# Kernel tuning notes

Measured on AMD Instinct MI355X. Metric: run time of the kernel, lower is better.

Reference implementation:

```python
import jax, jax.numpy as jnp
import numpy as np

B, DIM, NX, NY = 4, 64, 256, 256
HEADS, DIM_HEAD, LATENT, DIM_OUT, KM = 4, 32, 128, 64, 2
DH = DIM_HEAD * KM  # LowRankKernel head dim (also RoPE dim) = 64
EPS = 1e-5
MIN_FREQ = 1.0 / 64.0  # RotaryEmbedding default in FactFormer/LNS repo


def _gelu(x):
    return jax.nn.gelu(x, approximate=False)  # torch nn.GELU default (erf)


def _conv1x1(u, w):
    # u: [b,c,h,w], w: [out,c]  (1x1 conv == channel matmul)
    return jnp.einsum('bchw,oc->bohw', u, w)


def _pooling_reducer(x, win, ln_g, ln_b, w1, w2, b2):
    # x: [b, n_keep, n_pool, c] -> Linear, mean-pool over n_pool, LN+FFN
    h = jnp.einsum('bnmc,hc->bnmh', x, win).mean(axis=2)  # [b, n, hid]
    m = h.mean(axis=-1, keepdims=True)
    v = h.var(axis=-1, keepdims=True)
    h = (h - m) / jnp.sqrt(v + EPS) * ln_g + ln_b
    return _gelu(h @ w1.T) @ w2.T + b2  # [b, n, latent]


def _rope_freqs(n):
    pos = jnp.linspace(0.0, 1.0, n) / MIN_FREQ  # scale/min_freq = 64
    inv = 1.0 / (10000.0 ** (jnp.arange(0, DH, 2, dtype=jnp.float32) / DH))
    f = pos[:, None] * inv[None, :]            # [n, DH//2]
    return jnp.concatenate([f, f], axis=-1)    # [n, DH]


def _apply_rope(x, f):
    # rotate_half = cat(-x2, x1) on half-split (FactFormer convention)
    d = x.shape[-1] // 2
    rot = jnp.concatenate([-x[..., d:], x[..., :d]], axis=-1)
    return x * jnp.cos(f) + rot * jnp.sin(f)


def _low_rank_kernel(x, wqk):
    # x: [b, n, latent] -> K: [b, heads, n, n]; scaling=1, dropout=Identity, qk_norm=False
    b, n, _ = x.shape
    qk = x @ wqk.T
    q, k = jnp.split(qk, 2, axis=-1)
    q = q.reshape(b, n, HEADS, DH).transpose(0, 2, 1, 3)
    k = k.reshape(b, n, HEADS, DH).transpose(0, 2, 1, 3)
    f = _rope_freqs(n)
    q = _apply_rope(q, f)
    k = _apply_rope(k, f)
    return jnp.einsum('bhid,bhjd->bhij', q, k)


def _forward(u, gn_w, gn_b, w_in_proj, w_to_in,
             px_win, px_ln_g, px_ln_b, px_w1, px_w2, px_b2,
             py_win, py_ln_g, py_ln_b, py_w1, py_w2, py_b2,
             kx_wqk, ky_wqk, out_w1, out_w2):
    # GroupNorm(1, dim): normalize over (C,H,W) per sample, affine
    m = u.mean(axis=(1, 2, 3), keepdims=True)
    v = u.var(axis=(1, 2, 3), keepdims=True)
    un = (u - m) / jnp.sqrt(v + EPS) * gn_w[None, :, None, None] + gn_b[None, :, None, None]
    u_phi = _conv1x1(un, w_in_proj)  # [b, heads*dim_head, nx, ny]
    ui = _conv1x1(un, w_to_in)       # [b, dim, nx, ny]
    # to_x: pool over ny -> tokens along nx; to_y: pool over nx -> tokens along ny
    ux = _pooling_reducer(ui.transpose(0, 2, 3, 1), px_win, px_ln_g, px_ln_b, px_w1, px_w2, px_b2)  # [b, nx, latent]
    uy = _pooling_reducer(ui.transpose(0, 3, 2, 1), py_win, py_ln_g, py_ln_b, py_w1, py_w2, py_b2)  # [b, ny, latent]
    kx = _low_rank_kernel(ux, kx_wqk)  # [b, h, nx, nx]
    ky = _low_rank_kernel(uy, ky_wqk)  # [b, h, ny, ny]
    b, hc, nx, ny = u_phi.shape
    up = u_phi.reshape(b, HEADS, hc // HEADS, nx, ny)
    up = jnp.einsum('bhij,bhcjm->bhcim', kx, up)
    up = jnp.einsum('bhlm,bhcim->bhcil', ky, up)
    up = up.reshape(b, hc, nx, ny)
    # InstanceNorm2d (no affine, no running stats)
    m2 = up.mean(axis=(2, 3), keepdims=True)
    v2 = up.var(axis=(2, 3), keepdims=True)
    upn = (up - m2) / jnp.sqrt(v2 + EPS)
    out = _conv1x1(_gelu(_conv1x1(upn, out_w1)), out_w2)
    return out + u


def setup_inputs() -> dict:
    key = jax.random.key(0)
    ks = jax.random.split(key, 16)
    def w(k, shape, s=0.02):
        return (jax.random.normal(k, shape) * s).astype(jnp.float32)
    return {
        'u': jax.random.normal(ks[0], (B, DIM, NX, NY), dtype=jnp.float32),
        'gn_w': jnp.ones((DIM,), jnp.float32), 'gn_b': jnp.zeros((DIM,), jnp.float32),
        'w_in_proj': w(ks[1], (HEADS * DIM_HEAD, DIM)),
        'w_to_in': w(ks[2], (DIM, DIM)),
        'px_win': w(ks[3], (DIM, DIM)),
        'px_ln_g': jnp.ones((DIM,), jnp.float32), 'px_ln_b': jnp.zeros((DIM,), jnp.float32),
        'px_w1': w(ks[4], (2 * DIM, DIM)), 'px_w2': w(ks[5], (LATENT, 2 * DIM)),
        'px_b2': jnp.zeros((LATENT,), jnp.float32),
        'py_win': w(ks[6], (DIM, DIM)),
        'py_ln_g': jnp.ones((DIM,), jnp.float32), 'py_ln_b': jnp.zeros((DIM,), jnp.float32),
        'py_w1': w(ks[7], (2 * DIM, DIM)), 'py_w2': w(ks[8], (LATENT, 2 * DIM)),
        'py_b2': jnp.zeros((LATENT,), jnp.float32),
        'kx_wqk': w(ks[9], (2 * HEADS * DH, LATENT)),
        'ky_wqk': w(ks[10], (2 * HEADS * DH, LATENT)),
        'out_w1': w(ks[11], (DIM_OUT, HEADS * DIM_HEAD)),
        'out_w2': w(ks[12], (DIM_OUT, DIM_OUT)),
    }


def reference(u, gn_w, gn_b, w_in_proj, w_to_in,
              px_win, px_ln_g, px_ln_b, px_w1, px_w2, px_b2,
              py_win, py_ln_g, py_ln_b, py_w1, py_w2, py_b2,
              kx_wqk, ky_wqk, out_w1, out_w2):
    return _forward(u, gn_w, gn_b, w_in_proj, w_to_in,
                    px_win, px_ln_g, px_ln_b, px_w1, px_w2, px_b2,
                    py_win, py_ln_g, py_ln_b, py_w1, py_w2, py_b2,
                    kx_wqk, ky_wqk, out_w1, out_w2)
```

## Files before the change

kernel.cpp:

```cpp
#include <hip/hip_runtime.h>
#include <math.h>

typedef unsigned short ushort_t;
typedef unsigned int uint_t;
typedef __attribute__((ext_vector_type(8))) short s8v;
typedef __attribute__((ext_vector_type(4))) float f4;

#define NPIX 65536
#define EPS_ 1e-5f

__device__ __forceinline__ float bf2f(ushort_t u){ return __uint_as_float(((uint_t)u)<<16); }
__device__ __forceinline__ ushort_t f2bf(float f){
  uint_t u = __float_as_uint(f);
  uint_t r = (u + 0x7fffu + ((u>>16)&1u)) >> 16;
  return (ushort_t)r;
}
__device__ __forceinline__ float bflo(uint_t p){ return __uint_as_float(p<<16); }
__device__ __forceinline__ float bfhi(uint_t p){ return __uint_as_float(p & 0xffff0000u); }
__device__ __forceinline__ uint_t packbf(float a, float b){ return (uint_t)f2bf(a) | ((uint_t)f2bf(b)<<16); }

__device__ __forceinline__ f4 MFMA(s8v a, s8v b, f4 c){
  return __builtin_amdgcn_mfma_f32_16x16x32_bf16(a, b, c, 0, 0, 0);
}

__device__ __forceinline__ float wave_sum(float v){
  #pragma unroll
  for(int m=32;m>=1;m>>=1) v += __shfl_xor(v, m, 64);
  return v;
}

__global__ __launch_bounds__(256) void k1_stats(const float* __restrict__ u,
    float* __restrict__ part, float* __restrict__ pc, float* __restrict__ poolx){
  int blk = blockIdx.x; int b = blk>>8; int c = (blk>>2)&63; int iq = blk&3;
  int t = threadIdx.x; int lane = t&63; int w = t>>6;
  const float* up = u + ((size_t)(b*64+c))*NPIX + iq*64*256;
  __shared__ float sCol[4][256];
  __shared__ float red[8];
  float4 cs4 = {0.f,0.f,0.f,0.f};
  float ss = 0.f;
  #pragma unroll 4
  for(int r16=0;r16<16;r16++){
    int r = w*16 + r16;
    float4 v = *(const float4*)(up + r*256 + lane*4);
    cs4.x+=v.x; cs4.y+=v.y; cs4.z+=v.z; cs4.w+=v.w;
    ss += v.x*v.x+v.y*v.y+v.z*v.z+v.w*v.w;
    float rs = wave_sum(v.x+v.y+v.z+v.w);
    if(lane==0) poolx[(b*256 + iq*64 + r)*64 + c] = rs*(1.f/256.f);
  }
  *(float4*)&sCol[w][lane*4] = cs4;
  float ssw = wave_sum(ss);
  if(lane==0) red[w] = ssw;
  __syncthreads();
  float colsum = sCol[0][t]+sCol[1][t]+sCol[2][t]+sCol[3][t];
  pc[((b*64+c)*4+iq)*256 + t] = colsum;
  float s1 = wave_sum(colsum);
  if(lane==0) red[4+w] = s1;
  __syncthreads();
  if(t==0){
    part[((b*64+c)*4+iq)*2]   = red[4]+red[5]+red[6]+red[7];
    part[((b*64+c)*4+iq)*2+1] = red[0]+red[1]+red[2]+red[3];
  }
}

__global__ void k2_fin(const float* __restrict__ part, float* __restrict__ gnmv){
  int t = threadIdx.x; int b = t>>6; int i = t&63;
  float S1=0.f, S2=0.f;
  #pragma unroll
  for(int q=0;q<4;q++){
    S1 += part[((b*64+i)*4+q)*2];
    S2 += part[((b*64+i)*4+q)*2+1];
  }
  S1 = wave_sum(S1); S2 = wave_sum(S2);
  if(i==0){
    const float inv = 1.f/4194304.f;
    float m = S1*inv; float v = S2*inv - m*m;
    gnmv[b*2] = m; gnmv[b*2+1] = rsqrtf(v + EPS_);
  }
}

__global__ __launch_bounds__(256) void k8a_fold(const float* __restrict__ gnmv,
    const float* __restrict__ gnw, const float* __restrict__ gnb,
    const float* __restrict__ w_in_proj, const float* __restrict__ out_w2,
    ushort_t* __restrict__ wpb, float* __restrict__ c0g, ushort_t* __restrict__ w2b){
  int b = blockIdx.x; int t = threadIdx.x;
  __shared__ float scs[64], shs[64];
  if(t<64){
    float mean = gnmv[b*2], rstd = gnmv[b*2+1];
    float sc = rstd*gnw[t];
    scs[t] = sc; shs[t] = gnb[t] - mean*sc;
  }
  __syncthreads();
  int oc = t>>1, h = t&1;
  float c0 = 0.f;
  for(int k=0;k<32;k++){
    int ch = h*32 + k;
    float wv = w_in_proj[oc*64 + ch];
    wpb[((size_t)b*128 + oc)*64 + ch] = f2bf(wv*scs[ch]);
    c0 += wv*shs[ch];
  }
  c0 += __shfl_xor(c0, 1, 64);
  if(h==0) c0g[b*128 + oc] = c0;
  if(b==0){
    for(int e=t;e<4096;e+=256) w2b[e] = f2bf(out_w2[e]);
  }
}

__global__ void k8b_fold(const float* __restrict__ istat,
    const float* __restrict__ out_w1, ushort_t* __restrict__ W1b,
    float* __restrict__ bias1){
  int b = blockIdx.x; int t = threadIdx.x;
  __shared__ float ms[128], rss[128];
  ms[t] = istat[(b*128+t)*2];       rss[t] = istat[(b*128+t)*2+1];
  ms[64+t] = istat[(b*128+64+t)*2]; rss[64+t] = istat[(b*128+64+t)*2+1];
  __syncthreads();
  float bias = 0.f;
  for(int ch=0;ch<128;ch++){
    float wv = out_w1[t*128 + ch];
    float wr = wv*rss[ch];
    W1b[((size_t)b*64 + t)*128 + ch] = f2bf(wr);
    bias += wr*ms[ch];
  }
  bias1[b*64 + t] = bias;
}

__global__ __launch_bounds__(128) void k3_reduce(
    const float* __restrict__ poolx, const float* __restrict__ pc,
    const float* __restrict__ gnmv,
    const float* __restrict__ gnw, const float* __restrict__ gnb,
    const float* __restrict__ w_to_in,
    const float* __restrict__ xwin, const float* __restrict__ xlg, const float* __restrict__ xlb,
    const float* __restrict__ xw1, const float* __restrict__ xw2, const float* __restrict__ xb2,
    const float* __restrict__ ywin, const float* __restrict__ ylg, const float* __restrict__ ylb,
    const float* __restrict__ yw1, const float* __restrict__ yw2, const float* __restrict__ yb2,
    float* __restrict__ ux, float* __restrict__ uy){
  int id = blockIdx.x;
  int side = id >> 10; int r = id & 1023; int b = r>>8; int i = r&255;
  const float* win = side ? ywin : xwin;
  const float* lg  = side ? ylg  : xlg;
  const float* lb  = side ? ylb  : xlb;
  const float* w1  = side ? yw1  : xw1;
  const float* w2  = side ? yw2  : xw2;
  const float* b2  = side ? yb2  : xb2;
  float* outp = side ? uy : ux;
  int t = threadIdx.x;
  __shared__ float pn[64], t1[64], hh[64], f1[128];
  float mean = gnmv[b*2], rstd = gnmv[b*2+1];
  if(t<64){
    float pv;
    if(side){
      const float* p = pc + ((size_t)(b*64+t)*4)*256 + i;
      pv = (p[0] + p[256] + p[512] + p[768]) * (1.f/256.f);
    } else {
      pv = poolx[(b*256+i)*64 + t];
    }
    pn[t] = (pv - mean)*rstd*gnw[t] + gnb[t];
  }
  __syncthreads();
  if(t<64){
    float acc=0.f; const float* wr = w_to_in + t*64;
    #pragma unroll 8
    for(int c=0;c<64;c++) acc += pn[c]*wr[c];
    t1[t]=acc;
  }
  __syncthreads();
  if(t<64){
    float acc=0.f; const float* wr = win + t*64;
    #pragma unroll 8
    for(int c=0;c<64;c++) acc += t1[c]*wr[c];
    hh[t]=acc;
  }
  __syncthreads();
  if(t<64){
    float v = hh[t];
    float s = wave_sum(v);
    float ss = wave_sum(v*v);
    float m2 = s*(1.f/64.f);
    float var = ss*(1.f/64.f) - m2*m2;
    float rs2 = rsqrtf(var + EPS_);
    hh[t] = (v - m2)*rs2*lg[t] + lb[t];
  }
  __syncthreads();
  {
    float acc=0.f; const float* wr = w1 + t*64;
    #pragma unroll 8
    for(int c=0;c<64;c++) acc += hh[c]*wr[c];
    f1[t] = 0.5f*acc*(1.f + erff(acc*0.70710678118654752f));
  }
  __syncthreads();
  {
    float acc=0.f; const float* wr = w2 + t*128;
    #pragma unroll 8
    for(int j=0;j<128;j++) acc += f1[j]*wr[j];
    outp[(b*256+i)*128 + t] = acc + b2[t];
  }
}

__global__ __launch_bounds__(256) void k4_gemm(
    const float* __restrict__ ux, const float* __restrict__ uy,
    const float* __restrict__ wqkx, const float* __restrict__ wqky,
    ushort_t* __restrict__ qxb, ushort_t* __restrict__ kxTb,
    ushort_t* __restrict__ qyb, ushort_t* __restrict__ kyTb){
  int blk = blockIdx.x;
  int nt = blk&3; int mt = (blk>>2)&1; int b = (blk>>3)&3; int side = blk>>5;
  const float* x  = (side? uy:ux) + (size_t)(b*256 + mt*128)*128;
  const float* wq = (side? wqky:wqkx) + (size_t)nt*128*128;
  ushort_t* qb  = side? qyb : qxb;
  ushort_t* kTb = side? kyTb : kxTb;

  __shared__ __align__(16) ushort_t sA[128*136];
  __shared__ __align__(16) ushort_t sB[128*136];

  int t = threadIdx.x; int lane = t&63; int w = t>>6; int lr = lane&15; int lg = lane>>4;
  for(int e=t;e<4096;e+=256){
    int row = e>>5, c4 = (e&31)*4;
    float4 v = *(const float4*)(x + row*128 + c4);
    uint2 pk; pk.x = packbf(v.x,v.y); pk.y = packbf(v.z,v.w);
    *(uint2*)&sA[row*136 + c4] = pk;
    float4 wv = *(const float4*)(wq + row*128 + c4);
    uint2 wk; wk.x = packbf(wv.x,wv.y); wk.y = packbf(wv.z,wv.w);
    *(uint2*)&sB[row*136 + c4] = wk;
  }
  __syncthreads();
  const f4 fz = {0.f,0.f,0.f,0.f};
  f4 acc[2][8];
  #pragma unroll
  for(int it=0;it<2;it++)
    #pragma unroll
    for(int n2=0;n2<8;n2++) acc[it][n2]=fz;
  #pragma unroll
  for(int kc=0;kc<4;kc++){
    s8v bf[8];
    #pragma unroll
    for(int n2=0;n2<8;n2++)
      bf[n2] = *(const s8v*)&sB[(n2*16+lr)*136 + kc*32 + lg*8];
    #pragma unroll
    for(int it=0;it<2;it++){
      s8v a = *(const s8v*)&sA[(w*32+it*16+lr)*136 + kc*32 + lg*8];
      #pragma unroll
      for(int n2=0;n2<8;n2++)
        acc[it][n2] = MFMA(a, bf[n2], acc[it][n2]);
    }
  }
  if(nt < 2){
    #pragma unroll
    for(int it=0;it<2;it++){
      #pragma unroll
      for(int n2=0;n2<8;n2++){
        int o = nt*128 + n2*16 + lr;
        int h = o>>6, dd = o&63, t32 = dd&31;
        float invf = expf(-(float)t32*(9.210340371976184f/32.f));
        size_t base = (size_t)(b*4+h)*16384;
        #pragma unroll
        for(int r=0;r<4;r++){
          int i = mt*128 + w*32 + it*16 + lg*4 + r;
          float f = (64.f/255.f)*(float)i*invf;
          float sn, cs; __sincosf(f, &sn, &cs);
          float pair = acc[it][n2^2][r];
          float rot = ((n2&2)==0)? -pair : pair;
          float v = acc[it][n2][r]*cs + rot*sn;
          qb[base + (size_t)i*64 + dd] = f2bf(v);
        }
      }
    }
  } else {
    __syncthreads();
    #pragma unroll
    for(int it=0;it<2;it++){
      #pragma unroll
      for(int n2=0;n2<8;n2++){
        int ol = n2*16 + lr;
        int o = nt*128 + ol;
        int t32 = o&31;
        float invf = expf(-(float)t32*(9.210340371976184f/32.f));
        #pragma unroll
        for(int r=0;r<4;r++){
          int il = w*32 + it*16 + lg*4 + r;
          int i = mt*128 + il;
          float f = (64.f/255.f)*(float)i*invf;
          float sn, cs; __sincosf(f, &sn, &cs);
          float pair = acc[it][n2^2][r];
          float rot = ((n2&2)==0)? -pair : pair;
          float v = acc[it][n2][r]*cs + rot*sn;
          sA[ol*136 + il] = f2bf(v);
        }
      }
    }
    __syncthreads();
    {
      int row = t>>1, half = t&1;
      int h = (nt-2)*2 + (row>>6), dd = row&63;
      ushort_t* dst = kTb + (size_t)(b*4+h)*16384 + (size_t)dd*256 + mt*128 + half*64;
      const ushort_t* src = &sA[row*136 + half*64];
      #pragma unroll
      for(int j=0;j<8;j++)
        *(uint4*)(dst + j*8) = *(const uint4*)(src + j*8);
    }
  }
}

__global__ __launch_bounds__(256) void k5s_sums(const ushort_t* __restrict__ kxTb,
    const ushort_t* __restrict__ kyTb, float* __restrict__ ksum){
  int bh = blockIdx.x; int t = threadIdx.x;
  int row = t>>2, g = t&3;
  const ushort_t* kx = kxTb + (size_t)bh*16384 + row*256 + g*64;
  float s = 0.f;
  #pragma unroll
  for(int j=0;j<8;j++){
    uint4 v = *(const uint4*)(kx + j*8);
    s += bflo(v.x)+bfhi(v.x)+bflo(v.y)+bfhi(v.y)+bflo(v.z)+bfhi(v.z)+bflo(v.w)+bfhi(v.w);
  }
  s += __shfl_xor(s,1,64); s += __shfl_xor(s,2,64);
  if(g==0) ksum[bh*128 + row] = s;
  const ushort_t* ky = kyTb + (size_t)bh*16384 + row*256 + g*64;
  float s2 = 0.f;
  #pragma unroll
  for(int j=0;j<8;j++){
    uint4 v = *(const uint4*)(ky + j*8);
    s2 += bflo(v.x)+bfhi(v.x)+bflo(v.y)+bfhi(v.y)+bflo(v.z)+bfhi(v.z)+bflo(v.w)+bfhi(v.w);
  }
  s2 += __shfl_xor(s2,1,64); s2 += __shfl_xor(s2,2,64);
  if(g==0) ksum[bh*128 + 64 + row] = s2;
}

__global__ __launch_bounds__(512) void k7a_core(
    const float* __restrict__ u,
    const ushort_t* __restrict__ kxTb, const ushort_t* __restrict__ kyTb,
    ushort_t* __restrict__ Cb){
  int blk = blockIdx.x; int b = blk>>6;
  const float* up = u + (size_t)blk*NPIX;
  __shared__ __align__(16) ushort_t su[2][64*264];
  __shared__ __align__(16) ushort_t sT1[4][64*68];
  int t = threadIdx.x; int w = t>>6; int lane = t&63; int lr = lane&15; int lg = lane>>4;
  int h = w>>1, sub = w&1;
  const ushort_t* KyT = kyTb + (size_t)(b*4+h)*16384;
  const ushort_t* KxT = kxTb + (size_t)(b*4+h)*16384;
  const f4 fz = {0.f,0.f,0.f,0.f};
  f4 cacc[2][4];
  #pragma unroll
  for(int it=0;it<2;it++)
    #pragma unroll
    for(int et=0;et<4;et++) cacc[it][et]=fz;

  auto stageld = [&](int jc, int buf){
    #pragma unroll
    for(int k=0;k<8;k++){
      int flat = k*512 + t;
      int row = flat>>6, col4 = flat&63;
      float4 v = *(const float4*)(up + (size_t)(jc*64+row)*256 + col4*4);
      uint2 pk; pk.x = packbf(v.x,v.y); pk.y = packbf(v.z,v.w);
      *(uint2*)&su[buf][row*264 + col4*4] = pk;
    }
  };
  stageld(0, 0);
  __syncthreads();
  for(int jc=0;jc<4;jc++){
    int cur = jc&1;
    f4 acc[2][4];
    #pragma unroll
    for(int jt=0;jt<2;jt++)
      #pragma unroll
      for(int et=0;et<4;et++) acc[jt][et]=fz;
    #pragma unroll
    for(int km=0;km<8;km++){
      s8v a0 = *(const s8v*)&su[cur][(sub*32+lr)*264 + km*32 + lg*8];
      s8v a1 = *(const s8v*)&su[cur][(sub*32+16+lr)*264 + km*32 + lg*8];
      #pragma unroll
      for(int et=0;et<4;et++){
        s8v bv = *(const s8v*)(KyT + (et*16+lr)*256 + km*32 + lg*8);
        acc[0][et] = MFMA(a0,bv,acc[0][et]);
        acc[1][et] = MFMA(a1,bv,acc[1][et]);
      }
    }
    #pragma unroll
    for(int jt=0;jt<2;jt++)
      #pragma unroll
      for(int et=0;et<4;et++){
        f4 v = acc[jt][et];
        uint2 pk; pk.x=packbf(v.x,v.y); pk.y=packbf(v.z,v.w);
        *(uint2*)&sT1[h][(et*16+lr)*68 + sub*32 + jt*16 + lg*4] = pk;
      }
    __syncthreads();
    if(jc<3) stageld(jc+1, cur^1);
    #pragma unroll
    for(int kj=0;kj<2;kj++){
      s8v a0 = *(const s8v*)(KxT + (size_t)(sub*32+lr)*256 + jc*64 + kj*32 + lg*8);
      s8v a1 = *(const s8v*)(KxT + (size_t)(sub*32+16+lr)*256 + jc*64 + kj*32 + lg*8);
      #pragma unroll
      for(int et=0;et<4;et++){
        s8v bv = *(const s8v*)&sT1[h][(et*16+lr)*68 + kj*32 + lg*8];
        cacc[0][et] = MFMA(a0,bv,cacc[0][et]);
        cacc[1][et] = MFMA(a1,bv,cacc[1][et]);
      }
    }
    __syncthreads();
  }
  ushort_t* cbase = Cb + ((size_t)blk*4 + h)*4096;
  #pragma unroll
  for(int it=0;it<2;it++)
    #pragma unroll
    for(int et=0;et<4;et++){
      f4 v = cacc[it][et];
      uint2 pk; pk.x=packbf(v.x,v.y); pk.y=packbf(v.z,v.w);
      *(uint2*)&cbase[(et*16+lr)*64 + sub*32 + it*16 + lg*4] = pk;
    }
}

__global__ __launch_bounds__(256) void k7m_mix(
    const ushort_t* __restrict__ Cb, const ushort_t* __restrict__ wpb,
    const float* __restrict__ c0g, const float* __restrict__ ksum,
    ushort_t* __restrict__ cT){
  int blk = blockIdx.x; int bh = blk>>4; int et = blk&15;
  int b = bh>>2, h = bh&3;
  __shared__ __align__(16) ushort_t sC[64*264];
  __shared__ float sWf[32*64];
  __shared__ float sKx[64], sKy4[4];
  int t = threadIdx.x;
  #pragma unroll
  for(int k=0;k<8;k++){
    int flat = k*256 + t;
    int ic = flat>>5, q = flat&31;
    uint4 v = *(const uint4*)(Cb + ((size_t)(b*64+ic)*4 + h)*4096 + et*256 + q*8);
    *(uint4*)&sC[ic*264 + q*8] = v;
  }
  for(int e=t;e<2048;e+=256){
    int ch = e>>6, ic = e&63;
    sWf[e] = bf2f(wpb[((size_t)b*128 + h*32 + ch)*64 + ic]);
  }
  if(t<64) sKx[t] = ksum[bh*128 + t];
  if(t<4)  sKy4[t] = ksum[bh*128 + 64 + et*4 + t];
  __syncthreads();
  int chg = t>>5, edq = t&31, ed0 = edq*8;
  float c0v[4];
  #pragma unroll
  for(int cc=0;cc<4;cc++) c0v[cc] = c0g[b*128 + h*32 + chg*4 + cc];
  float acc[4][8];
  #pragma unroll
  for(int j=0;j<8;j++){
    int ed = ed0 + j;
    float r1 = sKy4[ed>>6]*sKx[ed&63];
    #pragma unroll
    for(int cc=0;cc<4;cc++) acc[cc][j] = c0v[cc]*r1;
  }
  for(int ic=0;ic<64;ic++){
    uint4 cv = *(const uint4*)&sC[ic*264 + ed0];
    float x[8];
    x[0]=bflo(cv.x); x[1]=bfhi(cv.x); x[2]=bflo(cv.y); x[3]=bfhi(cv.y);
    x[4]=bflo(cv.z); x[5]=bfhi(cv.z); x[6]=bflo(cv.w); x[7]=bfhi(cv.w);
    #pragma unroll
    for(int cc=0;cc<4;cc++){
      float wv = sWf[(chg*4+cc)*64 + ic];
      #pragma unroll
      for(int j=0;j<8;j++) acc[cc][j] += wv*x[j];
    }
  }
  #pragma unroll
  for(int cc=0;cc<4;cc++){
    uint2 p0, p1;
    p0.x = packbf(acc[cc][0],acc[cc][1]); p0.y = packbf(acc[cc][2],acc[cc][3]);
    p1.x = packbf(acc[cc][4],acc[cc][5]); p1.y = packbf(acc[cc][6],acc[cc][7]);
    ushort_t* dst = cT + ((size_t)bh*32 + chg*4+cc)*4096 + et*256 + ed0;
    *(uint2*)(dst) = p0;
    *(uint2*)(dst+4) = p1;
  }
}

__global__ __launch_bounds__(256) void k7b_heavy(
    const ushort_t* __restrict__ cT,
    const ushort_t* __restrict__ qxb, const ushort_t* __restrict__ qyb,
    ushort_t* __restrict__ up2, float* __restrict__ istat){
  int blk = blockIdx.x;
  int c = blk & 31; int h = (blk>>5)&3; int b = blk>>7;
  int bh = b*4 + h; int ch = h*32 + c;
  const ushort_t* Qx  = qxb + (size_t)bh*16384;
  const ushort_t* Qy  = qyb + (size_t)bh*16384;
  const ushort_t* cTc = cT + (size_t)(bh*32 + c)*4096;
  ushort_t* out_c = up2 + (size_t)(b*128 + ch)*NPIX;

  __shared__ __align__(16) ushort_t sP[256*72];
  __shared__ float sRed[8];

  int t = threadIdx.x; int w = t>>6; int lane = t&63; int lr = lane&15; int lg = lane>>4;
  const f4 fz = {0.f,0.f,0.f,0.f};
  {
    s8v aF[4][2];
    #pragma unroll
    for(int me=0;me<4;me++)
      #pragma unroll
      for(int kd=0;kd<2;kd++)
        aF[me][kd] = *(const s8v*)(cTc + (me*16+lr)*64 + kd*32 + lg*8);
    #pragma unroll
    for(int it=0;it<4;it++){
      s8v b0 = *(const s8v*)(Qx + (w*64+it*16+lr)*64 + lg*8);
      s8v b1 = *(const s8v*)(Qx + (w*64+it*16+lr)*64 + 32 + lg*8);
      #pragma unroll
      for(int me=0;me<4;me++){
        f4 pv = MFMA(aF[me][0], b0, fz);
        pv = MFMA(aF[me][1], b1, pv);
        uint2 pk; pk.x=packbf(pv.x,pv.y); pk.y=packbf(pv.z,pv.w);
        *(uint2*)&sP[(w*64+it*16+lr)*72 + me*16 + lg*4] = pk;
      }
    }
  }
  __syncthreads();
  float lsum=0.f, lssq=0.f;
  {
    s8v aP[4][2];
    #pragma unroll
    for(int it=0;it<4;it++)
      #pragma unroll
      for(int ke=0;ke<2;ke++)
        aP[it][ke] = *(const s8v*)&sP[(w*64+it*16+lr)*72 + ke*32 + lg*8];
    for(int lt=0;lt<4;lt++){
      s8v bq[4][2];
      #pragma unroll
      for(int nt=0;nt<4;nt++)
        #pragma unroll
        for(int ke=0;ke<2;ke++)
          bq[nt][ke] = *(const s8v*)(Qy + (lt*64+nt*16+lr)*64 + ke*32 + lg*8);
      #pragma unroll
      for(int it=0;it<4;it++){
        #pragma unroll
        for(int nt=0;nt<4;nt++){
          f4 o = MFMA(bq[nt][0], aP[it][0], fz);
          o = MFMA(bq[nt][1], aP[it][1], o);
          lsum += o[0]+o[1]+o[2]+o[3];
          lssq += o[0]*o[0]+o[1]*o[1]+o[2]*o[2]+o[3]*o[3];
          uint2 pk; pk.x = packbf(o[0],o[1]); pk.y = packbf(o[2],o[3]);
          *(uint2*)(out_c + (size_t)(w*64 + it*16 + lr)*256 + lt*64 + nt*16 + lg*4) = pk;
        }
      }
    }
  }
  float a1 = wave_sum(lsum), a2 = wave_sum(lssq);
  if(lane==0){ sRed[w]=a1; sRed[4+w]=a2; }
  __syncthreads();
  if(t==0){
    float S = sRed[0]+sRed[1]+sRed[2]+sRed[3];
    float SS = sRed[4]+sRed[5]+sRed[6]+sRed[7];
    float m = S*(1.f/65536.f);
    float var = SS*(1.f/65536.f) - m*m;
    istat[(b*128+ch)*2] = m;
    istat[(b*128+ch)*2+1] = rsqrtf(var + EPS_);
  }
}

__global__ __launch_bounds__(256) void kf_out(
    const ushort_t* __restrict__ up2, const ushort_t* __restrict__ W1b,
    const float* __restrict__ bias1, const ushort_t* __restrict__ w2b,
    const float* __restrict__ u, float* __restrict__ out){
  int blk = blockIdx.x;
  int b = blk>>9; int pix0 = (blk&511)<<7;
  __shared__ __align__(16) unsigned char smraw[128*132*2];
  ushort_t* sX = (ushort_t*)smraw;
  ushort_t* sG = (ushort_t*)smraw;
  float* sO = (float*)smraw;
  int t = threadIdx.x; int lane = t&63; int w = t>>6; int lr = lane&15; int lg = lane>>4;
  {
    int ch = t>>4; int px = (t&15)*8;
    #pragma unroll
    for(int it=0; it<8; it++){
      int c = it*16 + ch;
      uint4 v = *(const uint4*)(up2 + ((size_t)(b*128+c))*NPIX + pix0 + px);
      uint2 lo; lo.x = v.x; lo.y = v.y;
      uint2 hi; hi.x = v.z; hi.y = v.w;
      *(uint2*)&sX[c*132 + px] = lo;
      *(uint2*)&sX[c*132 + px + 4] = hi;
    }
  }
  __syncthreads();
  const ushort_t* w1p = W1b + (size_t)b*64*128;
  f4 g[2][4];
  #pragma unroll
  for(int it=0;it<2;it++)
    #pragma unroll
    for(int nt=0;nt<4;nt++){
      float bv = -bias1[b*64 + nt*16 + lr];
      f4 ci = {bv,bv,bv,bv};
      g[it][nt] = ci;
    }
  #pragma unroll
  for(int kc=0;kc<4;kc++){
    s8v bf[4];
    #pragma unroll
    for(int nt=0;nt<4;nt++)
      bf[nt] = *(const s8v*)(w1p + (nt*16+lr)*128 + kc*32 + lg*8);
    #pragma unroll
    for(int it=0;it<2;it++){
      int pix = w*32 + it*16 + lr;
      s8v a;
      #pragma unroll
      for(int j=0;j<8;j++) a[j] = (short)sX[(kc*32+lg*8+j)*132 + pix];
      #pragma unroll
      for(int nt=0;nt<4;nt++)
        g[it][nt] = MFMA(a, bf[nt], g[it][nt]);
    }
  }
  #pragma unroll
  for(int it=0;it<2;it++)
    #pragma unroll
    for(int nt=0;nt<4;nt++){
      f4 v = g[it][nt];
      #pragma unroll
      for(int r=0;r<4;r++){
        float x = v[r];
        v[r] = 0.5f*x*(1.f + erff(x*0.70710678118654752f));
      }
      g[it][nt] = v;
    }
  __syncthreads();
  #pragma unroll
  for(int it=0;it<2;it++)
    #pragma unroll
    for(int nt=0;nt<4;nt++){
      f4 v = g[it][nt];
      uint2 pk; pk.x = packbf(v.x,v.y); pk.y = packbf(v.z,v.w);
      *(uint2*)&sG[(nt*16+lr)*132 + w*32 + it*16 + lg*4] = pk;
    }
  __syncthreads();
  f4 o2[2][4];
  const f4 fz = {0.f,0.f,0.f,0.f};
  #pragma unroll
  for(int it=0;it<2;it++)
    #pragma unroll
    for(int nt=0;nt<4;nt++) o2[it][nt]=fz;
  #pragma unroll
  for(int kc=0;kc<2;kc++){
    s8v bf[4];
    #pragma unroll
    for(int nt=0;nt<4;nt++)
      bf[nt] = *(const s8v*)(w2b + (nt*16+lr)*64 + kc*32 + lg*8);
    #pragma unroll
    for(int it=0;it<2;it++){
      int pix = w*32 + it*16 + lr;
      s8v a;
      #pragma unroll
      for(int j=0;j<8;j++) a[j] = (short)sG[(kc*32+lg*8+j)*132 + pix];
      #pragma unroll
      for(int nt=0;nt<4;nt++)
        o2[it][nt] = MFMA(a, bf[nt], o2[it][nt]);
    }
  }
  __syncthreads();
  #pragma unroll
  for(int it=0;it<2;it++)
    #pragma unroll
    for(int nt=0;nt<4;nt++)
      *(f4*)&sO[(nt*16+lr)*132 + w*32 + it*16 + lg*4] = o2[it][nt];
  __syncthreads();
  {
    int oc = t>>5; int px = (t&31)*4;
    #pragma unroll
    for(int it=0;it<8;it++){
      int o = it*8 + oc;
      float4 ov = *(const float4*)&sO[o*132 + px];
      float4 uv = *(const float4*)(u + ((size_t)(b*64+o))*NPIX + pix0 + px);
      float4 rv;
      rv.x = ov.x+uv.x; rv.y = ov.y+uv.y; rv.z = ov.z+uv.z; rv.w = ov.w+uv.w;
      *(float4*)(out + ((size_t)(b*64+o))*NPIX + pix0 + px) = rv;
    }
  }
}

extern "C" void kernel_launch(void* const* d_in, const int* in_sizes, int n_in,
                              void* d_out, int out_size, void* d_ws, size_t ws_size,
                              hipStream_t stream) {
  (void)in_sizes; (void)n_in; (void)out_size; (void)ws_size;
  const float* u        = (const float*)d_in[0];
  const float* gnw      = (const float*)d_in[1];
  const float* gnb      = (const float*)d_in[2];
  const float* w_in_proj= (const float*)d_in[3];
  const float* w_to_in  = (const float*)d_in[4];
  const float* px_win   = (const float*)d_in[5];
  const float* px_ln_g  = (const float*)d_in[6];
  const float* px_ln_b  = (const float*)d_in[7];
  const float* px_w1    = (const float*)d_in[8];
  const float* px_w2    = (const float*)d_in[9];
  const float* px_b2    = (const float*)d_in[10];
  const float* py_win   = (const float*)d_in[11];
  const float* py_ln_g  = (const float*)d_in[12];
  const float* py_ln_b  = (const float*)d_in[13];
  const float* py_w1    = (const float*)d_in[14];
  const float* py_w2    = (const float*)d_in[15];
  const float* py_b2    = (const float*)d_in[16];
  const float* kx_wqk   = (const float*)d_in[17];
  const float* ky_wqk   = (const float*)d_in[18];
  const float* out_w1   = (const float*)d_in[19];
  const float* out_w2   = (const float*)d_in[20];
  float* out = (float*)d_out;

  float* fw = (float*)d_ws;
  float* part  = fw + 0;
  float* gnmv  = fw + 2048;
  float* pc    = fw + 4096;
  float* poolx = fw + 266240;
  float* ux    = fw + 397312;
  float* uy    = fw + 528384;
  float* istat = fw + 659456;
  float* c0g   = fw + 660480;
  float* bias1 = fw + 660992;
  ushort_t* wpb = (ushort_t*)(fw + 661504);
  ushort_t* W1b = (ushort_t*)(fw + 677888);
  ushort_t* w2b = (ushort_t*)(fw + 694272);
  float* ksum   = fw + 696320;
  ushort_t* qxb  = (ushort_t*)(fw + 4096);
  ushort_t* kxTb = (ushort_t*)(fw + 135168);
  ushort_t* qyb  = (ushort_t*)(fw + 698368);
  ushort_t* kyTb = (ushort_t*)(fw + 829440);
  ushort_t* up2  = (ushort_t*)(fw + 960512);
  ushort_t* Cb = (ushort_t*)d_out;
  ushort_t* cT = (ushort_t*)d_out + 4194304;

  k1_stats<<<dim3(1024), dim3(256), 0, stream>>>(u, part, pc, poolx);
  k2_fin<<<dim3(1), dim3(256), 0, stream>>>(part, gnmv);
  k8a_fold<<<dim3(4), dim3(256), 0, stream>>>(gnmv, gnw, gnb, w_in_proj, out_w2, wpb, c0g, w2b);
  k3_reduce<<<dim3(2048), dim3(128), 0, stream>>>(poolx, pc, gnmv, gnw, gnb, w_to_in,
      px_win, px_ln_g, px_ln_b, px_w1, px_w2, px_b2,
      py_win, py_ln_g, py_ln_b, py_w1, py_w2, py_b2, ux, uy);
  k4_gemm<<<dim3(64), dim3(256), 0, stream>>>(ux, uy, kx_wqk, ky_wqk, qxb, kxTb, qyb, kyTb);
  k5s_sums<<<dim3(16), dim3(256), 0, stream>>>(kxTb, kyTb, ksum);
  k7a_core<<<dim3(256), dim3(512), 0, stream>>>(u, kxTb, kyTb, Cb);
  k7m_mix<<<dim3(256), dim3(256), 0, stream>>>(Cb, wpb, c0g, ksum, cT);
  k7b_heavy<<<dim3(512), dim3(256), 0, stream>>>(cT, qxb, qyb, up2, istat);
  k8b_fold<<<dim3(4), dim3(64), 0, stream>>>(istat, out_w1, W1b, bias1);
  kf_out<<<dim3(2048), dim3(256), 0, stream>>>(up2, W1b, bias1, w2b, u, out);
}
```

Before: 201.1 us.

## Fold GroupNorm finalize into weight-fold kernel and rewrite pooling reducer with MFMA

```diff
diff --git a/kernel.cpp b/kernel.cpp
--- a/kernel.cpp
+++ b/kernel.cpp
@@ -62,32 +62,33 @@
   }
 }
 
-__global__ void k2_fin(const float* __restrict__ part, float* __restrict__ gnmv){
-  int t = threadIdx.x; int b = t>>6; int i = t&63;
-  float S1=0.f, S2=0.f;
-  #pragma unroll
-  for(int q=0;q<4;q++){
-    S1 += part[((b*64+i)*4+q)*2];
-    S2 += part[((b*64+i)*4+q)*2+1];
-  }
-  S1 = wave_sum(S1); S2 = wave_sum(S2);
-  if(i==0){
-    const float inv = 1.f/4194304.f;
-    float m = S1*inv; float v = S2*inv - m*m;
-    gnmv[b*2] = m; gnmv[b*2+1] = rsqrtf(v + EPS_);
-  }
-}
-
-__global__ __launch_bounds__(256) void k8a_fold(const float* __restrict__ gnmv,
+__global__ __launch_bounds__(256) void k8a_fold(const float* __restrict__ part,
     const float* __restrict__ gnw, const float* __restrict__ gnb,
     const float* __restrict__ w_in_proj, const float* __restrict__ out_w2,
-    ushort_t* __restrict__ wpb, float* __restrict__ c0g, ushort_t* __restrict__ w2b){
+    float* __restrict__ gnmv, ushort_t* __restrict__ wpb,
+    float* __restrict__ c0g, ushort_t* __restrict__ w2b){
   int b = blockIdx.x; int t = threadIdx.x;
-  __shared__ float scs[64], shs[64];
+  __shared__ float scs[64], shs[64], sMV[2];
   if(t<64){
-    float mean = gnmv[b*2], rstd = gnmv[b*2+1];
-    float sc = rstd*gnw[t];
-    scs[t] = sc; shs[t] = gnb[t] - mean*sc;
+    float S1=0.f, S2=0.f;
+    #pragma unroll
+    for(int q=0;q<4;q++){
+      S1 += part[((b*64+t)*4+q)*2];
+      S2 += part[((b*64+t)*4+q)*2+1];
+    }
+    S1 = wave_sum(S1); S2 = wave_sum(S2);
+    if(t==0){
+      const float inv = 1.f/4194304.f;
+      float m = S1*inv; float v = S2*inv - m*m;
+      float rs = rsqrtf(v + EPS_);
+      gnmv[b*2] = m; gnmv[b*2+1] = rs;
+      sMV[0] = m; sMV[1] = rs;
+    }
+  }
+  __syncthreads();
+  if(t<64){
+    float sc = sMV[1]*gnw[t];
+    scs[t] = sc; shs[t] = gnb[t] - sMV[0]*sc;
   }
   __syncthreads();
   int oc = t>>1, h = t&1;
@@ -123,7 +124,7 @@
   bias1[b*64 + t] = bias;
 }
 
-__global__ __launch_bounds__(128) void k3_reduce(
+__global__ __launch_bounds__(256) void k3_mfma(
     const float* __restrict__ poolx, const float* __restrict__ pc,
     const float* __restrict__ gnmv,
     const float* __restrict__ gnw, const float* __restrict__ gnb,
@@ -133,65 +134,217 @@
     const float* __restrict__ ywin, const float* __restrict__ ylg, const float* __restrict__ ylb,
     const float* __restrict__ yw1, const float* __restrict__ yw2, const float* __restrict__ yb2,
     float* __restrict__ ux, float* __restrict__ uy){
-  int id = blockIdx.x;
-  int side = id >> 10; int r = id & 1023; int b = r>>8; int i = r&255;
+  int blk = blockIdx.x;
+  int side = blk>>3; int b = (blk>>1)&3; int mt = blk&1;
+  int i0 = mt*128;
   const float* win = side ? ywin : xwin;
-  const float* lg  = side ? ylg  : xlg;
-  const float* lb  = side ? ylb  : xlb;
+  const float* lnw = side ? ylg  : xlg;
+  const float* lnb = side ? ylb  : xlb;
   const float* w1  = side ? yw1  : xw1;
   const float* w2  = side ? yw2  : xw2;
   const float* b2  = side ? yb2  : xb2;
   float* outp = side ? uy : ux;
-  int t = threadIdx.x;
-  __shared__ float pn[64], t1[64], hh[64], f1[128];
-  float mean = gnmv[b*2], rstd = gnmv[b*2+1];
-  if(t<64){
-    float pv;
-    if(side){
-      const float* p = pc + ((size_t)(b*64+t)*4)*256 + i;
-      pv = (p[0] + p[256] + p[512] + p[768]) * (1.f/256.f);
+
+  __shared__ __align__(16) ushort_t sA[128*136];
+  __shared__ __align__(16) ushort_t sB[128*136];
+  __shared__ __align__(16) ushort_t sW[128*136];
+  __shared__ float sGw[64], sGb[64], sLg[64], sLb[64];
+  float* sF = (float*)sA;
+
+  int t = threadIdx.x; int lane = t&63; int w = t>>6; int lr = lane&15; int lgq = lane>>4;
+  const f4 fz = {0.f,0.f,0.f,0.f};
+
+  if(t<64){ sGw[t]=gnw[t]; sGb[t]=gnb[t]; sLg[t]=lnw[t]; sLb[t]=lnb[t]; }
+  for(int e=t;e<2048;e+=256){
+    int r = e>>5, c2 = e&31;
+    *(uint_t*)&sW[r*136 + c2*2] = packbf(w_to_in[r*64 + c2*2], w_to_in[r*64 + c2*2 + 1]);
+  }
+  __syncthreads();
+  {
+    float mean = gnmv[b*2], rstd = gnmv[b*2+1];
+    int chalf = t>>7, tok = t&127;
+    if(side==0){
+      const float* pb = poolx + ((size_t)(b*256 + i0 + tok))*64 + chalf*32;
+      #pragma unroll 8
+      for(int cc=0;cc<32;cc++){
+        int c = chalf*32+cc;
+        float pn = (pb[cc]-mean)*rstd*sGw[c] + sGb[c];
+        sA[c*136 + tok] = f2bf(pn);
+      }
     } else {
-      pv = poolx[(b*256+i)*64 + t];
-    }
-    pn[t] = (pv - mean)*rstd*gnw[t] + gnb[t];
-  }
-  __syncthreads();
-  if(t<64){
-    float acc=0.f; const float* wr = w_to_in + t*64;
+      #pragma unroll 4
+      for(int cc=0;cc<32;cc++){
+        int c = chalf*32+cc;
+        const float* p = pc + ((size_t)(b*64+c)*4)*256 + (i0+tok);
+        float pv = (p[0]+p[256]+p[512]+p[768])*(1.f/256.f);
+        float pn = (pv-mean)*rstd*sGw[c] + sGb[c];
+        sA[c*136 + tok] = f2bf(pn);
+      }
+    }
+  }
+  __syncthreads();
+  {
+    f4 acc[2][4];
+    #pragma unroll
+    for(int it=0;it<2;it++)
+      #pragma unroll
+      for(int nt=0;nt<4;nt++) acc[it][nt]=fz;
+    #pragma unroll
+    for(int kc=0;kc<2;kc++){
+      s8v bf[4];
+      #pragma unroll
+      for(int nt=0;nt<4;nt++)
+        bf[nt] = *(const s8v*)&sW[(nt*16+lr)*136 + kc*32 + lgq*8];
+      #pragma unroll
+      for(int it=0;it<2;it++){
+        int tok = w*32 + it*16 + lr;
+        s8v a;
+        #pragma unroll
+        for(int j=0;j<8;j++) a[j] = (short)sA[(kc*32+lgq*8+j)*136 + tok];
+        #pragma unroll
+        for(int nt=0;nt<4;nt++)
+          acc[it][nt] = MFMA(a, bf[nt], acc[it][nt]);
+      }
+    }
+    __syncthreads();
+    #pragma unroll
+    for(int it=0;it<2;it++)
+      #pragma unroll
+      for(int nt=0;nt<4;nt++){
+        f4 v = acc[it][nt];
+        uint2 pk; pk.x = packbf(v.x,v.y); pk.y = packbf(v.z,v.w);
+        *(uint2*)&sB[(nt*16+lr)*136 + w*32 + it*16 + lgq*4] = pk;
+      }
+  }
+  for(int e=t;e<2048;e+=256){
+    int r = e>>5, c2 = e&31;
+    *(uint_t*)&sW[r*136 + c2*2] = packbf(win[r*64 + c2*2], win[r*64 + c2*2 + 1]);
+  }
+  __syncthreads();
+  {
+    f4 acc[2][4];
+    #pragma unroll
+    for(int it=0;it<2;it++)
+      #pragma unroll
+      for(int nt=0;nt<4;nt++) acc[it][nt]=fz;
+    #pragma unroll
+    for(int kc=0;kc<2;kc++){
+      s8v bf[4];
+      #pragma unroll
+      for(int nt=0;nt<4;nt++)
+        bf[nt] = *(const s8v*)&sW[(nt*16+lr)*136 + kc*32 + lgq*8];
+      #pragma unroll
+      for(int it=0;it<2;it++){
+        int tok = w*32 + it*16 + lr;
+        s8v a;
+        #pragma unroll
+        for(int j=0;j<8;j++) a[j] = (short)sB[(kc*32+lgq*8+j)*136 + tok];
+        #pragma unroll
+        for(int nt=0;nt<4;nt++)
+          acc[it][nt] = MFMA(bf[nt], a, acc[it][nt]);
+      }
+    }
+    __syncthreads();
+    #pragma unroll
+    for(int it=0;it<2;it++)
+      #pragma unroll
+      for(int nt=0;nt<4;nt++)
+        *(f4*)&sF[(size_t)(w*32+it*16+lr)*68 + nt*16 + lgq*4] = acc[it][nt];
+  }
+  __syncthreads();
+  for(int e=t;e<4096;e+=256){
+    int r = e>>5, c2 = e&31;
+    *(uint_t*)&sW[r*136 + c2*2] = packbf(w1[r*64 + c2*2], w1[r*64 + c2*2 + 1]);
+  }
+  if(t<128){
+    float s=0.f, ss=0.f;
     #pragma unroll 8
-    for(int c=0;c<64;c++) acc += pn[c]*wr[c];
-    t1[t]=acc;
-  }
-  __syncthreads();
-  if(t<64){
-    float acc=0.f; const float* wr = win + t*64;
-    #pragma unroll 8
-    for(int c=0;c<64;c++) acc += t1[c]*wr[c];
-    hh[t]=acc;
-  }
-  __syncthreads();
-  if(t<64){
-    float v = hh[t];
-    float s = wave_sum(v);
-    float ss = wave_sum(v*v);
+    for(int o=0;o<64;o++){ float v = sF[(size_t)t*68 + o]; s+=v; ss+=v*v; }
     float m2 = s*(1.f/64.f);
     float var = ss*(1.f/64.f) - m2*m2;
     float rs2 = rsqrtf(var + EPS_);
-    hh[t] = (v - m2)*rs2*lg[t] + lb[t];
+    #pragma unroll 8
+    for(int o=0;o<64;o++){
+      float lnv = (sF[(size_t)t*68 + o]-m2)*rs2*sLg[o] + sLb[o];
+      sB[o*136 + t] = f2bf(lnv);
+    }
   }
   __syncthreads();
   {
-    float acc=0.f; const float* wr = w1 + t*64;
-    #pragma unroll 8
-    for(int c=0;c<64;c++) acc += hh[c]*wr[c];
-    f1[t] = 0.5f*acc*(1.f + erff(acc*0.70710678118654752f));
+    f4 acc[2][8];
+    #pragma unroll
+    for(int it=0;it<2;it++)
+      #pragma unroll
+      for(int nt=0;nt<8;nt++) acc[it][nt]=fz;
+    #pragma unroll
+    for(int kc=0;kc<2;kc++){
+      s8v bf[8];
+      #pragma unroll
+      for(int nt=0;nt<8;nt++)
+        bf[nt] = *(const s8v*)&sW[(nt*16+lr)*136 + kc*32 + lgq*8];
+      #pragma unroll
+      for(int it=0;it<2;it++){
+        int tok = w*32 + it*16 + lr;
+        s8v a;
+        #pragma unroll
+        for(int j=0;j<8;j++) a[j] = (short)sB[(kc*32+lgq*8+j)*136 + tok];
+        #pragma unroll
+        for(int nt=0;nt<8;nt++)
+          acc[it][nt] = MFMA(a, bf[nt], acc[it][nt]);
+      }
+    }
+    __syncthreads();
+    #pragma unroll
+    for(int it=0;it<2;it++)
+      #pragma unroll
+      for(int nt=0;nt<8;nt++){
+        f4 v = acc[it][nt];
+        #pragma unroll
+        for(int r=0;r<4;r++){
+          float x = v[r];
+          v[r] = 0.5f*x*(1.f + erff(x*0.70710678118654752f));
+        }
+        uint2 pk; pk.x = packbf(v[0],v[1]); pk.y = packbf(v[2],v[3]);
+        *(uint2*)&sA[(nt*16+lr)*136 + w*32 + it*16 + lgq*4] = pk;
+      }
+  }
+  __syncthreads();
+  for(int e=t;e<8192;e+=256){
+    int r = e>>6, c2 = e&63;
+    *(uint_t*)&sW[r*136 + c2*2] = packbf(w2[r*128 + c2*2], w2[r*128 + c2*2 + 1]);
   }
   __syncthreads();
   {
-    float acc=0.f; const float* wr = w2 + t*128;
-    #pragma unroll 8
-    for(int j=0;j<128;j++) acc += f1[j]*wr[j];
-    outp[(b*256+i)*128 + t] = acc + b2[t];
+    f4 acc[2][8];
+    #pragma unroll
+    for(int nt=0;nt<8;nt++){
+      f4 bb = *(const f4*)&b2[nt*16 + lgq*4];
+      acc[0][nt] = bb; acc[1][nt] = bb;
+    }
+    #pragma unroll
+    for(int kc=0;kc<4;kc++){
+      s8v bf[8];
+      #pragma unroll
+      for(int nt=0;nt<8;nt++)
+        bf[nt] = *(const s8v*)&sW[(nt*16+lr)*136 + kc*32 + lgq*8];
+      #pragma unroll
+      for(int it=0;it<2;it++){
+        int tok = w*32 + it*16 + lr;
+        s8v a;
+        #pragma unroll
+        for(int j=0;j<8;j++) a[j] = (short)sA[(kc*32+lgq*8+j)*136 + tok];
+        #pragma unroll
+        for(int nt=0;nt<8;nt++)
+          acc[it][nt] = MFMA(bf[nt], a, acc[it][nt]);
+      }
+    }
+    #pragma unroll
+    for(int it=0;it<2;it++){
+      int tok = w*32 + it*16 + lr;
+      #pragma unroll
+      for(int nt=0;nt<8;nt++)
+        *(f4*)&outp[((size_t)(b*256 + i0 + tok))*128 + nt*16 + lgq*4] = acc[it][nt];
+    }
   }
 }
 
@@ -711,9 +864,8 @@
   ushort_t* cT = (ushort_t*)d_out + 4194304;
 
   k1_stats<<<dim3(1024), dim3(256), 0, stream>>>(u, part, pc, poolx);
-  k2_fin<<<dim3(1), dim3(256), 0, stream>>>(part, gnmv);
-  k8a_fold<<<dim3(4), dim3(256), 0, stream>>>(gnmv, gnw, gnb, w_in_proj, out_w2, wpb, c0g, w2b);
-  k3_reduce<<<dim3(2048), dim3(128), 0, stream>>>(poolx, pc, gnmv, gnw, gnb, w_to_in,
+  k8a_fold<<<dim3(4), dim3(256), 0, stream>>>(part, gnw, gnb, w_in_proj, out_w2, gnmv, wpb, c0g, w2b);
+  k3_mfma<<<dim3(16), dim3(256), 0, stream>>>(poolx, pc, gnmv, gnw, gnb, w_to_in,
       px_win, px_ln_g, px_ln_b, px_w1, px_w2, px_b2,
       py_win, py_ln_g, py_ln_b, py_w1, py_w2, py_b2, ux, uy);
   k4_gemm<<<dim3(64), dim3(256), 0, stream>>>(ux, uy, kx_wqk, ky_wqk, qxb, kxTb, qyb, kyTb);
```

New measurement: 196.4 us (median of 2 runs). -2.3%, faster.
